# Kernel tuning notes

Hardware: AMD Instinct MI355X
Metric: run time of the kernel (lower is better)

The kernel has to match this reference:

```python
import jax, jax.numpy as jnp
import numpy as np

B, T, C = 2, 2048, 1024
N_HEAD, N_GROUP = 16, 4
N_KV = N_HEAD // N_GROUP          # 4
HEAD_DIM = C // N_HEAD            # 64
ROPE_BASE = 10000.0
INIT_STD = 0.02


def setup_inputs() -> dict:
    key = jax.random.key(0)
    ks = jax.random.split(key, 5)
    kvC = N_KV * HEAD_DIM
    return {
        "x": jax.random.normal(ks[0], (B, T, C), jnp.float32),
        "w_q": jax.random.normal(ks[1], (C, C), jnp.float32) * INIT_STD,
        "b_q": jnp.zeros((C,), jnp.float32),
        "w_k": jax.random.normal(ks[2], (C, kvC), jnp.float32) * INIT_STD,
        "b_k": jnp.zeros((kvC,), jnp.float32),
        "w_v": jax.random.normal(ks[3], (C, kvC), jnp.float32) * INIT_STD,
        "b_v": jnp.zeros((kvC,), jnp.float32),
        "w_o": jax.random.normal(ks[4], (C, C), jnp.float32) * INIT_STD,
        "b_o": jnp.zeros((C,), jnp.float32),
    }


def reference(x, w_q, b_q, w_k, b_k, w_v, b_v, w_o, b_o):
    Bx, Tx, Cx = x.shape
    # projections (torch Linear math with weights stored as [in, out])
    q = (x @ w_q + b_q).reshape(Bx, Tx, N_HEAD, HEAD_DIM).transpose(0, 2, 1, 3)  # [B,H,T,hd]
    k = (x @ w_k + b_k).reshape(Bx, Tx, N_KV, HEAD_DIM).transpose(0, 2, 1, 3)    # [B,KV,T,hd]
    v = (x @ w_v + b_v).reshape(Bx, Tx, N_KV, HEAD_DIM).transpose(0, 2, 1, 3)

    # RoPE with INTERLEAVED pair convention: pairs are (dim 2i, dim 2i+1)
    inv_freq = 1.0 / (ROPE_BASE ** (jnp.arange(0, HEAD_DIM, 2, dtype=jnp.float32) / HEAD_DIM))
    freqs = jnp.arange(Tx, dtype=jnp.float32)[:, None] * inv_freq[None, :]       # [T, hd/2]
    cos, sin = jnp.cos(freqs), jnp.sin(freqs)

    def rope(t):
        tp = t.reshape(*t.shape[:-1], HEAD_DIM // 2, 2)
        e, o = tp[..., 0], tp[..., 1]          # even/odd lanes, [B,h,T,hd/2]
        er = e * cos - o * sin
        orr = e * sin + o * cos
        return jnp.stack([er, orr], axis=-1).reshape(t.shape)

    q, k = rope(q), rope(k)

    # GQA: duplicate each KV head n_group times (consecutively, like repeat_interleave)
    k = jnp.repeat(k, N_GROUP, axis=1)   # [B,H,T,hd]
    v = jnp.repeat(v, N_GROUP, axis=1)

    attn = jnp.einsum('bhqd,bhkd->bhqk', q, k) / np.sqrt(HEAD_DIM).astype(np.float32)
    causal = jnp.tril(jnp.ones((Tx, Tx), bool))
    attn = jnp.where(causal, attn, -jnp.inf)
    attn = jax.nn.softmax(attn, axis=-1)

    out = jnp.einsum('bhqk,bhkd->bhqd', attn, v)            # [B,H,T,hd]
    out = out.transpose(0, 2, 1, 3).reshape(Bx, Tx, Cx)
    return out @ w_o + b_o
```

## Files before the change

### kernel.cpp

```cpp
#include <hip/hip_runtime.h>
#include <hip/hip_bf16.h>

typedef __hip_bfloat16 bf16;
typedef __attribute__((ext_vector_type(8))) short short8_t;
typedef __attribute__((ext_vector_type(4))) short short4_t;
typedef __attribute__((ext_vector_type(4))) float f32x4;

#define B_SZ   2
#define T_SEQ  2048
#define C_DIM  1024
#define NH     16
#define NKV    4
#define HD     64
#define QKVW   1536

#define LOG2_BASE_OVER_32 0.4152410118609203f
#define Q_SCALE 0.1803368801111204f

__device__ __forceinline__ short f2bs(float f) {
    unsigned u = __float_as_uint(f);
    u += 0x7FFFu + ((u >> 16) & 1u);
    return (short)(u >> 16);
}
__device__ __forceinline__ short f2bs_trunc(float f) {
    return (short)(__float_as_uint(f) >> 16);
}
__device__ __forceinline__ float bs2f(short s) {
    unsigned u = ((unsigned)(unsigned short)s) << 16;
    return __uint_as_float(u);
}

__device__ __forceinline__ void store_c(float* p, float v) { *p = v; }
__device__ __forceinline__ void store_c(short* p, float v) { *p = f2bs(v); }

__device__ __forceinline__ float dpp_max16(float x) {
    int t;
    t = __builtin_amdgcn_update_dpp(0, __float_as_int(x), 0xB1, 0xF, 0xF, true);
    x = fmaxf(x, __int_as_float(t));
    t = __builtin_amdgcn_update_dpp(0, __float_as_int(x), 0x4E, 0xF, 0xF, true);
    x = fmaxf(x, __int_as_float(t));
    t = __builtin_amdgcn_update_dpp(0, __float_as_int(x), 0x141, 0xF, 0xF, true);
    x = fmaxf(x, __int_as_float(t));
    t = __builtin_amdgcn_update_dpp(0, __float_as_int(x), 0x140, 0xF, 0xF, true);
    x = fmaxf(x, __int_as_float(t));
    return x;
}

__device__ __forceinline__ void transpose_tile(
    const float* __restrict__ W, short* __restrict__ Wt,
    int K, int N, int n0, int k0, int tid)
{
    __shared__ float tile[32][33];
    int tx = tid & 31, ty = tid >> 5;
    #pragma unroll
    for (int i = 0; i < 4; ++i)
        tile[ty + 8 * i][tx] = W[(size_t)(k0 + ty + 8 * i) * N + n0 + tx];
    __syncthreads();
    #pragma unroll
    for (int i = 0; i < 4; ++i)
        Wt[(size_t)(n0 + ty + 8 * i) * K + k0 + tx] = f2bs(tile[tx][ty + 8 * i]);
}

__global__ __launch_bounds__(256) void prep_kernel(
    const float* __restrict__ x,
    const float* __restrict__ w_q, const float* __restrict__ w_k,
    const float* __restrict__ w_v, const float* __restrict__ w_o,
    const float* __restrict__ b_q, const float* __restrict__ b_k,
    const float* __restrict__ b_v,
    short* __restrict__ Xb, short* __restrict__ Wqkv, short* __restrict__ Wto,
    float* __restrict__ Bqkv, float2* __restrict__ Tab)
{
    int blk = blockIdx.x, tid = threadIdx.x;
    if (blk < 4096) {
        int i = blk * 1024 + tid * 4;
        float4 v = *(const float4*)(x + i);
        short4_t o;
        o[0] = f2bs(v.x); o[1] = f2bs(v.y); o[2] = f2bs(v.z); o[3] = f2bs(v.w);
        *(short4_t*)(Xb + i) = o;
    } else if (blk < 5120) {
        int l = blk - 4096;
        transpose_tile(w_q, Wqkv, C_DIM, C_DIM, (l & 31) * 32, (l >> 5) * 32, tid);
    } else if (blk < 5376) {
        int l = blk - 5120;
        transpose_tile(w_k, Wqkv + (size_t)1024 * C_DIM, C_DIM, 256,
                       (l & 7) * 32, (l >> 3) * 32, tid);
    } else if (blk < 5632) {
        int l = blk - 5376;
        transpose_tile(w_v, Wqkv + (size_t)1280 * C_DIM, C_DIM, 256,
                       (l & 7) * 32, (l >> 3) * 32, tid);
    } else if (blk < 6656) {
        int l = blk - 5632;
        transpose_tile(w_o, Wto, C_DIM, C_DIM, (l & 31) * 32, (l >> 5) * 32, tid);
    } else if (blk < 6662) {
        int i = (blk - 6656) * 256 + tid;
        float v;
        if (i < 1024)      v = b_q[i];
        else if (i < 1280) v = b_k[i - 1024];
        else               v = b_v[i - 1280];
        Bqkv[i] = v;
    } else {
        int idx = (blk - 6662) * 256 + tid;
        int t = idx >> 5, i = idx & 31;
        float ang = (float)t * exp2f(-(float)i * LOG2_BASE_OVER_32);
        Tab[idx] = make_float2(cosf(ang), sinf(ang));
    }
}

template <typename CT>
__global__ __launch_bounds__(256) void gemm_mfma_bt(
    const short* __restrict__ A, const short* __restrict__ Bt,
    const float* __restrict__ bias, CT* __restrict__ C,
    int M, int N, int K)
{
    __shared__ __align__(16) short sA[2][128][40];
    __shared__ __align__(16) short sB[2][128][40];

    int m0 = blockIdx.y * 128;
    int n0 = blockIdx.x * 128;
    int tid  = threadIdx.x;
    int w    = tid >> 6, lane = tid & 63;
    int quad = lane >> 4, l16 = lane & 15;
    int wm = w & 1, wn = w >> 1;

    f32x4 acc[4][4] = {};

    short8_t ra[2], rb[2];
    #pragma unroll
    for (int it = 0; it < 2; ++it) {
        int slot = tid + 256 * it, row = slot >> 2, g = (slot & 3) * 8;
        ra[it] = *(const short8_t*)(A  + (size_t)(m0 + row) * K + g);
        rb[it] = *(const short8_t*)(Bt + (size_t)(n0 + row) * K + g);
    }

    int buf = 0;
    for (int k0 = 0; k0 < K; k0 += 32, buf ^= 1) {
        #pragma unroll
        for (int it = 0; it < 2; ++it) {
            int slot = tid + 256 * it, row = slot >> 2, g = (slot & 3) * 8;
            *(short8_t*)&sA[buf][row][g] = ra[it];
            *(short8_t*)&sB[buf][row][g] = rb[it];
        }
        if (k0 + 32 < K) {
            #pragma unroll
            for (int it = 0; it < 2; ++it) {
                int slot = tid + 256 * it, row = slot >> 2, g = (slot & 3) * 8;
                ra[it] = *(const short8_t*)(A  + (size_t)(m0 + row) * K + k0 + 32 + g);
                rb[it] = *(const short8_t*)(Bt + (size_t)(n0 + row) * K + k0 + 32 + g);
            }
        }
        __syncthreads();

        short8_t af[4], bfr[4];
        #pragma unroll
        for (int mt = 0; mt < 4; ++mt)
            af[mt] = *(const short8_t*)&sA[buf][wm * 64 + mt * 16 + l16][quad * 8];
        #pragma unroll
        for (int nt = 0; nt < 4; ++nt)
            bfr[nt] = *(const short8_t*)&sB[buf][wn * 64 + nt * 16 + l16][quad * 8];
        #pragma unroll
        for (int mt = 0; mt < 4; ++mt)
            #pragma unroll
            for (int nt = 0; nt < 4; ++nt)
                acc[mt][nt] = __builtin_amdgcn_mfma_f32_16x16x32_bf16(
                    af[mt], bfr[nt], acc[mt][nt], 0, 0, 0);
    }

    #pragma unroll
    for (int mt = 0; mt < 4; ++mt) {
        #pragma unroll
        for (int nt = 0; nt < 4; ++nt) {
            int col = n0 + wn * 64 + nt * 16 + l16;
            float bv = bias[col];
            #pragma unroll
            for (int r = 0; r < 4; ++r) {
                int row = m0 + wm * 64 + mt * 16 + quad * 4 + r;
                store_c(&C[(size_t)row * N + col], acc[mt][nt][r] + bv);
            }
        }
    }
}

__global__ __launch_bounds__(256) void rope_k_kernel(
    short* __restrict__ QKV, const float2* __restrict__ Tab)
{
    int g = blockIdx.x * 256 + threadIdx.x;
    int row = g >> 7, pi = g & 127;
    int col = 1024 + pi * 2;
    int t = row & (T_SEQ - 1);
    int i = pi & 31;

    size_t base = (size_t)row * QKVW + col;
    float e = bs2f(QKV[base]);
    float o = bs2f(QKV[base + 1]);

    float2 cs = Tab[t * 32 + i];

    QKV[base]     = f2bs(e * cs.x - o * cs.y);
    QKV[base + 1] = f2bs(e * cs.y + o * cs.x);
}

__global__ __launch_bounds__(256) void attn_mfma5(
    const short* __restrict__ QKV, const float2* __restrict__ Tab,
    short* __restrict__ O)
{
    __shared__ __align__(16) short sK [64][72];
    __shared__ __align__(16) short sVt[64][72];
    __shared__ __align__(16) short sP [4][16][72];

    const int tid  = threadIdx.x;
    const int w    = tid >> 6;
    const int lane = tid & 63;
    const int quad = lane >> 4;
    const int l16  = lane & 15;

    int blk = blockIdx.x;
    int grp = blk & 7;
    int tq  = 127 - (blk >> 3);
    int kvh = grp & 3;
    int b   = grp >> 2;
    int h   = kvh * 4 + w;
    int ct  = tq >> 2;

    const short* qptr = QKV + ((size_t)(b * T_SEQ + tq * 16 + l16)) * QKVW + h * HD;
    short8_t q0r = *(const short8_t*)(qptr + quad * 8);
    short8_t q1r = *(const short8_t*)(qptr + quad * 8 + 32);
    int t = tq * 16 + l16;
    const float2* tb = Tab + t * 32 + quad * 4;
    short8_t qf0, qf1;
    #pragma unroll
    for (int j = 0; j < 4; ++j) {
        float2 cs0 = tb[j];
        float e0 = bs2f(q0r[2 * j]), o0 = bs2f(q0r[2 * j + 1]);
        qf0[2 * j]     = f2bs((e0 * cs0.x - o0 * cs0.y) * Q_SCALE);
        qf0[2 * j + 1] = f2bs((e0 * cs0.y + o0 * cs0.x) * Q_SCALE);
        float2 cs1 = tb[j + 16];
        float e1 = bs2f(q1r[2 * j]), o1 = bs2f(q1r[2 * j + 1]);
        qf1[2 * j]     = f2bs((e1 * cs1.x - o1 * cs1.y) * Q_SCALE);
        qf1[2 * j + 1] = f2bs((e1 * cs1.y + o1 * cs1.x) * Q_SCALE);
    }

    const short* kbase = QKV + (size_t)b * T_SEQ * QKVW + 1024 + kvh * HD;
    const short* vbase = QKV + (size_t)b * T_SEQ * QKVW + 1280 + kvh * HD;

    short8_t ones;
    #pragma unroll
    for (int i = 0; i < 8; ++i) ones[i] = (short)0x3F80;

    float mrow[4], lrow[4];
    f32x4 oacc[4];
    #pragma unroll
    for (int r = 0; r < 4; ++r) { mrow[r] = -INFINITY; lrow[r] = 0.f; }
    #pragma unroll
    for (int dt = 0; dt < 4; ++dt) oacc[dt] = (f32x4){0.f, 0.f, 0.f, 0.f};

    const int kkey = tid >> 3, kd = (tid & 7) * 8;
    const int vkey = tid & 63, vd = (tid >> 6) * 8;

    short8_t kr[2], vr[2];
    #pragma unroll
    for (int it = 0; it < 2; ++it) {
        kr[it] = *(const short8_t*)(kbase + (size_t)(kkey + 32 * it) * QKVW + kd);
        vr[it] = *(const short8_t*)(vbase + (size_t)vkey * QKVW + vd + 32 * it);
    }

    for (int c = 0; c <= ct; ++c) {
        __syncthreads();
        #pragma unroll
        for (int it = 0; it < 2; ++it) {
            *(short8_t*)&sK[kkey + 32 * it][kd] = kr[it];
            #pragma unroll
            for (int i = 0; i < 8; ++i) sVt[vd + 32 * it + i][vkey] = vr[it][i];
        }
        __syncthreads();
        if (c < ct) {
            int jn = (c + 1) * 64;
            #pragma unroll
            for (int it = 0; it < 2; ++it) {
                kr[it] = *(const short8_t*)(kbase + (size_t)(jn + kkey + 32 * it) * QKVW + kd);
                vr[it] = *(const short8_t*)(vbase + (size_t)(jn + vkey) * QKVW + vd + 32 * it);
            }
        }

        f32x4 sacc[4];
        #pragma unroll
        for (int nt = 0; nt < 4; ++nt) {
            f32x4 z = {0.f, 0.f, 0.f, 0.f};
            short8_t kf0 = *(const short8_t*)&sK[l16 + 16 * nt][quad * 8];
            short8_t kf1 = *(const short8_t*)&sK[l16 + 16 * nt][quad * 8 + 32];
            z = __builtin_amdgcn_mfma_f32_16x16x32_bf16(qf0, kf0, z, 0, 0, 0);
            z = __builtin_amdgcn_mfma_f32_16x16x32_bf16(qf1, kf1, z, 0, 0, 0);
            sacc[nt] = z;
        }

        bool maskc = (c == ct);
        int j0 = c * 64;
        float al[4];
        #pragma unroll
        for (int r = 0; r < 4; ++r) {
            int trow = tq * 16 + quad * 4 + r;
            float sv[4], vmax = -INFINITY;
            #pragma unroll
            for (int nt = 0; nt < 4; ++nt) {
                float s = sacc[nt][r];
                if (maskc && (j0 + 16 * nt + l16 > trow)) s = -INFINITY;
                sv[nt] = s;
                vmax = fmaxf(vmax, s);
            }
            vmax = dpp_max16(vmax);
            float mnew = fmaxf(mrow[r], vmax);
            al[r] = exp2f(mrow[r] - mnew);
            mrow[r] = mnew;
            #pragma unroll
            for (int nt = 0; nt < 4; ++nt)
                sP[w][quad * 4 + r][16 * nt + l16] = f2bs_trunc(exp2f(sv[nt] - mnew));
        }
        if (__any((al[0] < 1.f) || (al[1] < 1.f) || (al[2] < 1.f) || (al[3] < 1.f))) {
            #pragma unroll
            for (int r = 0; r < 4; ++r) lrow[r] *= al[r];
            #pragma unroll
            for (int dt = 0; dt < 4; ++dt) {
                f32x4 o = oacc[dt];
                o[0] *= al[0]; o[1] *= al[1]; o[2] *= al[2]; o[3] *= al[3];
                oacc[dt] = o;
            }
        }

        short8_t pf0 = *(const short8_t*)&sP[w][l16][quad * 8];
        short8_t pf1 = *(const short8_t*)&sP[w][l16][quad * 8 + 32];
        f32x4 rs = {0.f, 0.f, 0.f, 0.f};
        rs = __builtin_amdgcn_mfma_f32_16x16x32_bf16(pf0, ones, rs, 0, 0, 0);
        rs = __builtin_amdgcn_mfma_f32_16x16x32_bf16(pf1, ones, rs, 0, 0, 0);
        #pragma unroll
        for (int r = 0; r < 4; ++r) lrow[r] += rs[r];
        #pragma unroll
        for (int dt = 0; dt < 4; ++dt) {
            short8_t vf0 = *(const short8_t*)&sVt[l16 + 16 * dt][quad * 8];
            short8_t vf1 = *(const short8_t*)&sVt[l16 + 16 * dt][quad * 8 + 32];
            oacc[dt] = __builtin_amdgcn_mfma_f32_16x16x32_bf16(pf0, vf0, oacc[dt], 0, 0, 0);
            oacc[dt] = __builtin_amdgcn_mfma_f32_16x16x32_bf16(pf1, vf1, oacc[dt], 0, 0, 0);
        }
    }

    #pragma unroll
    for (int r = 0; r < 4; ++r) {
        int m = quad * 4 + r;
        float inv = __builtin_amdgcn_rcpf(lrow[r]);
        #pragma unroll
        for (int dt = 0; dt < 4; ++dt)
            O[((size_t)b * T_SEQ + tq * 16 + m) * C_DIM + h * HD + 16 * dt + l16] =
                f2bs(oacc[dt][r] * inv);
    }
}

extern "C" void kernel_launch(void* const* d_in, const int* in_sizes, int n_in,
                              void* d_out, int out_size, void* d_ws, size_t ws_size,
                              hipStream_t stream)
{
    const float* x   = (const float*)d_in[0];
    const float* w_q = (const float*)d_in[1];
    const float* b_q = (const float*)d_in[2];
    const float* w_k = (const float*)d_in[3];
    const float* b_k = (const float*)d_in[4];
    const float* w_v = (const float*)d_in[5];
    const float* b_v = (const float*)d_in[6];
    const float* w_o = (const float*)d_in[7];
    const float* b_o = (const float*)d_in[8];
    float* out = (float*)d_out;

    char* ws = (char*)d_ws;
    short*  Xb   = (short*) (ws);
    short*  Ab   = (short*) (ws + ((size_t)8  << 20));
    short*  QKVb = (short*) (ws + ((size_t)16 << 20));
    short*  Wqkv = (short*) (ws + ((size_t)28 << 20));
    short*  Wto  = (short*) (ws + ((size_t)31 << 20));
    float*  Bqkv = (float*) (ws + ((size_t)33 << 20));
    float2* Tab  = (float2*)(ws + ((size_t)33 << 20) + 8192);

    const int M = B_SZ * T_SEQ;

    prep_kernel<<<6918, 256, 0, stream>>>(
        x, w_q, w_k, w_v, w_o, b_q, b_k, b_v, Xb, Wqkv, Wto, Bqkv, Tab);

    gemm_mfma_bt<short><<<dim3(QKVW / 128, M / 128), 256, 0, stream>>>(
        Xb, Wqkv, Bqkv, QKVb, M, QKVW, C_DIM);

    rope_k_kernel<<<2048, 256, 0, stream>>>(QKVb, Tab);

    attn_mfma5<<<B_SZ * NKV * 128, 256, 0, stream>>>(QKVb, Tab, Ab);

    gemm_mfma_bt<float><<<dim3(C_DIM / 128, M / 128), 256, 0, stream>>>(
        Ab, Wto, b_o, out, M, C_DIM, C_DIM);
}
```

Measured before the change: 190.3 us.

## Pre-transpose V globally and compute transposed scores to simplify softmax

The RoPE-K kernel now also writes a transposed copy of V to workspace. The attention kernel can then fill its V tile in shared memory with plain vector stores instead of scalar transposing writes. The score MFMA swaps its operands so each lane holds one query's scores across keys. This makes the row max and sum a two-step shuffle per lane, and removes the ones-vector MFMA row sum and the DPP reductions. In exchange it adds an extra global V transpose pass and cross-lane shuffles to broadcast the rescale factors.

```diff
diff --git a/kernel.cpp b/kernel.cpp
--- a/kernel.cpp
+++ b/kernel.cpp
@@ -32,19 +32,6 @@
 
 __device__ __forceinline__ void store_c(float* p, float v) { *p = v; }
 __device__ __forceinline__ void store_c(short* p, float v) { *p = f2bs(v); }
-
-__device__ __forceinline__ float dpp_max16(float x) {
-    int t;
-    t = __builtin_amdgcn_update_dpp(0, __float_as_int(x), 0xB1, 0xF, 0xF, true);
-    x = fmaxf(x, __int_as_float(t));
-    t = __builtin_amdgcn_update_dpp(0, __float_as_int(x), 0x4E, 0xF, 0xF, true);
-    x = fmaxf(x, __int_as_float(t));
-    t = __builtin_amdgcn_update_dpp(0, __float_as_int(x), 0x141, 0xF, 0xF, true);
-    x = fmaxf(x, __int_as_float(t));
-    t = __builtin_amdgcn_update_dpp(0, __float_as_int(x), 0x140, 0xF, 0xF, true);
-    x = fmaxf(x, __int_as_float(t));
-    return x;
-}
 
 __device__ __forceinline__ void transpose_tile(
     const float* __restrict__ W, short* __restrict__ Wt,
@@ -180,28 +167,50 @@
     }
 }
 
-__global__ __launch_bounds__(256) void rope_k_kernel(
-    short* __restrict__ QKV, const float2* __restrict__ Tab)
-{
-    int g = blockIdx.x * 256 + threadIdx.x;
-    int row = g >> 7, pi = g & 127;
-    int col = 1024 + pi * 2;
-    int t = row & (T_SEQ - 1);
-    int i = pi & 31;
-
-    size_t base = (size_t)row * QKVW + col;
-    float e = bs2f(QKV[base]);
-    float o = bs2f(QKV[base + 1]);
-
-    float2 cs = Tab[t * 32 + i];
-
-    QKV[base]     = f2bs(e * cs.x - o * cs.y);
-    QKV[base + 1] = f2bs(e * cs.y + o * cs.x);
-}
-
-__global__ __launch_bounds__(256) void attn_mfma5(
-    const short* __restrict__ QKV, const float2* __restrict__ Tab,
-    short* __restrict__ O)
+__global__ __launch_bounds__(256) void rope_k_transpose_v(
+    short* __restrict__ QKV, const float2* __restrict__ Tab,
+    short* __restrict__ Vt)
+{
+    int blk = blockIdx.x, tid = threadIdx.x;
+    if (blk < 2048) {
+        int g = blk * 256 + tid;
+        int row = g >> 7, pi = g & 127;
+        int col = 1024 + pi * 2;
+        int t = row & (T_SEQ - 1);
+        int i = pi & 31;
+        size_t base = (size_t)row * QKVW + col;
+        float e = bs2f(QKV[base]);
+        float o = bs2f(QKV[base + 1]);
+        float2 cs = Tab[t * 32 + i];
+        QKV[base]     = f2bs(e * cs.x - o * cs.y);
+        QKV[base + 1] = f2bs(e * cs.y + o * cs.x);
+    } else {
+        __shared__ __align__(16) short sT[64][72];
+        int l = blk - 2048;
+        int d0 = (l >> 6) * 64;
+        int r0 = (l & 63) * 64;
+        int i0 = tid >> 3, seg = (tid & 7) * 8;
+        #pragma unroll
+        for (int it = 0; it < 2; ++it) {
+            int i = i0 + 32 * it;
+            *(short8_t*)&sT[i][seg] =
+                *(const short8_t*)(QKV + (size_t)(r0 + i) * QKVW + 1280 + d0 + seg);
+        }
+        __syncthreads();
+        #pragma unroll
+        for (int it = 0; it < 2; ++it) {
+            int d = i0 + 32 * it;
+            short8_t o;
+            #pragma unroll
+            for (int k = 0; k < 8; ++k) o[k] = sT[seg + k][d];
+            *(short8_t*)(Vt + (size_t)(d0 + d) * (B_SZ * T_SEQ) + r0 + seg) = o;
+        }
+    }
+}
+
+__global__ __launch_bounds__(256) void attn_mfma6(
+    const short* __restrict__ QKV, const short* __restrict__ Vt,
+    const float2* __restrict__ Tab, short* __restrict__ O)
 {
     __shared__ __align__(16) short sK [64][72];
     __shared__ __align__(16) short sVt[64][72];
@@ -224,8 +233,8 @@
     const short* qptr = QKV + ((size_t)(b * T_SEQ + tq * 16 + l16)) * QKVW + h * HD;
     short8_t q0r = *(const short8_t*)(qptr + quad * 8);
     short8_t q1r = *(const short8_t*)(qptr + quad * 8 + 32);
-    int t = tq * 16 + l16;
-    const float2* tb = Tab + t * 32 + quad * 4;
+    int tg = tq * 16 + l16;
+    const float2* tb = Tab + tg * 32 + quad * 4;
     short8_t qf0, qf1;
     #pragma unroll
     for (int j = 0; j < 4; ++j) {
@@ -239,37 +248,30 @@
         qf1[2 * j + 1] = f2bs((e1 * cs1.y + o1 * cs1.x) * Q_SCALE);
     }
 
-    const short* kbase = QKV + (size_t)b * T_SEQ * QKVW + 1024 + kvh * HD;
-    const short* vbase = QKV + (size_t)b * T_SEQ * QKVW + 1280 + kvh * HD;
-
-    short8_t ones;
-    #pragma unroll
-    for (int i = 0; i < 8; ++i) ones[i] = (short)0x3F80;
-
-    float mrow[4], lrow[4];
+    const short* kbase  = QKV + (size_t)b * T_SEQ * QKVW + 1024 + kvh * HD;
+    const short* vtbase = Vt + (size_t)(kvh * HD) * (B_SZ * T_SEQ) + b * T_SEQ;
+
+    float m_l = -INFINITY, l_l = 0.f;
     f32x4 oacc[4];
     #pragma unroll
-    for (int r = 0; r < 4; ++r) { mrow[r] = -INFINITY; lrow[r] = 0.f; }
-    #pragma unroll
     for (int dt = 0; dt < 4; ++dt) oacc[dt] = (f32x4){0.f, 0.f, 0.f, 0.f};
 
     const int kkey = tid >> 3, kd = (tid & 7) * 8;
-    const int vkey = tid & 63, vd = (tid >> 6) * 8;
+    const int vdim = tid >> 3, vseg = (tid & 7) * 8;
 
     short8_t kr[2], vr[2];
     #pragma unroll
     for (int it = 0; it < 2; ++it) {
         kr[it] = *(const short8_t*)(kbase + (size_t)(kkey + 32 * it) * QKVW + kd);
-        vr[it] = *(const short8_t*)(vbase + (size_t)vkey * QKVW + vd + 32 * it);
+        vr[it] = *(const short8_t*)(vtbase + (size_t)(vdim + 32 * it) * (B_SZ * T_SEQ) + vseg);
     }
 
     for (int c = 0; c <= ct; ++c) {
         __syncthreads();
         #pragma unroll
         for (int it = 0; it < 2; ++it) {
-            *(short8_t*)&sK[kkey + 32 * it][kd] = kr[it];
-            #pragma unroll
-            for (int i = 0; i < 8; ++i) sVt[vd + 32 * it + i][vkey] = vr[it][i];
+            *(short8_t*)&sK [kkey + 32 * it][kd]   = kr[it];
+            *(short8_t*)&sVt[vdim + 32 * it][vseg] = vr[it];
         }
         __syncthreads();
         if (c < ct) {
@@ -277,65 +279,72 @@
             #pragma unroll
             for (int it = 0; it < 2; ++it) {
                 kr[it] = *(const short8_t*)(kbase + (size_t)(jn + kkey + 32 * it) * QKVW + kd);
-                vr[it] = *(const short8_t*)(vbase + (size_t)(jn + vkey) * QKVW + vd + 32 * it);
+                vr[it] = *(const short8_t*)(vtbase + (size_t)(vdim + 32 * it) * (B_SZ * T_SEQ) + jn + vseg);
             }
         }
 
         f32x4 sacc[4];
         #pragma unroll
-        for (int nt = 0; nt < 4; ++nt) {
+        for (int kt = 0; kt < 4; ++kt) {
             f32x4 z = {0.f, 0.f, 0.f, 0.f};
-            short8_t kf0 = *(const short8_t*)&sK[l16 + 16 * nt][quad * 8];
-            short8_t kf1 = *(const short8_t*)&sK[l16 + 16 * nt][quad * 8 + 32];
-            z = __builtin_amdgcn_mfma_f32_16x16x32_bf16(qf0, kf0, z, 0, 0, 0);
-            z = __builtin_amdgcn_mfma_f32_16x16x32_bf16(qf1, kf1, z, 0, 0, 0);
-            sacc[nt] = z;
-        }
-
-        bool maskc = (c == ct);
-        int j0 = c * 64;
-        float al[4];
-        #pragma unroll
-        for (int r = 0; r < 4; ++r) {
-            int trow = tq * 16 + quad * 4 + r;
-            float sv[4], vmax = -INFINITY;
-            #pragma unroll
-            for (int nt = 0; nt < 4; ++nt) {
-                float s = sacc[nt][r];
-                if (maskc && (j0 + 16 * nt + l16 > trow)) s = -INFINITY;
-                sv[nt] = s;
-                vmax = fmaxf(vmax, s);
+            short8_t kf0 = *(const short8_t*)&sK[l16 + 16 * kt][quad * 8];
+            short8_t kf1 = *(const short8_t*)&sK[l16 + 16 * kt][quad * 8 + 32];
+            z = __builtin_amdgcn_mfma_f32_16x16x32_bf16(kf0, qf0, z, 0, 0, 0);
+            z = __builtin_amdgcn_mfma_f32_16x16x32_bf16(kf1, qf1, z, 0, 0, 0);
+            sacc[kt] = z;
+        }
+
+        if (c == ct) {
+            int j0 = c * 64;
+            #pragma unroll
+            for (int kt = 0; kt < 4; ++kt)
+                #pragma unroll
+                for (int r = 0; r < 4; ++r)
+                    if (j0 + 16 * kt + quad * 4 + r > tg) sacc[kt][r] = -INFINITY;
+        }
+
+        float vmax = sacc[0][0];
+        #pragma unroll
+        for (int kt = 0; kt < 4; ++kt)
+            #pragma unroll
+            for (int r = 0; r < 4; ++r) vmax = fmaxf(vmax, sacc[kt][r]);
+        vmax = fmaxf(vmax, __shfl_xor(vmax, 16));
+        vmax = fmaxf(vmax, __shfl_xor(vmax, 32));
+        float mnew = fmaxf(m_l, vmax);
+        float al = exp2f(m_l - mnew);
+        m_l = mnew;
+
+        float psum = 0.f;
+        #pragma unroll
+        for (int kt = 0; kt < 4; ++kt) {
+            short4_t pk;
+            #pragma unroll
+            for (int r = 0; r < 4; ++r) {
+                float p = exp2f(sacc[kt][r] - mnew);
+                psum += p;
+                pk[r] = f2bs_trunc(p);
             }
-            vmax = dpp_max16(vmax);
-            float mnew = fmaxf(mrow[r], vmax);
-            al[r] = exp2f(mrow[r] - mnew);
-            mrow[r] = mnew;
-            #pragma unroll
-            for (int nt = 0; nt < 4; ++nt)
-                sP[w][quad * 4 + r][16 * nt + l16] = f2bs_trunc(exp2f(sv[nt] - mnew));
-        }
-        if (__any((al[0] < 1.f) || (al[1] < 1.f) || (al[2] < 1.f) || (al[3] < 1.f))) {
-            #pragma unroll
-            for (int r = 0; r < 4; ++r) lrow[r] *= al[r];
-            #pragma unroll
-            for (int dt = 0; dt < 4; ++dt) {
-                f32x4 o = oacc[dt];
-                o[0] *= al[0]; o[1] *= al[1]; o[2] *= al[2]; o[3] *= al[3];
-                oacc[dt] = o;
+            *(short4_t*)&sP[w][l16][16 * kt + 4 * quad] = pk;
+        }
+        psum += __shfl_xor(psum, 16);
+        psum += __shfl_xor(psum, 32);
+        l_l = l_l * al + psum;
+
+        if (__any(al < 1.f)) {
+            #pragma unroll
+            for (int r = 0; r < 4; ++r) {
+                float alr = __shfl(al, quad * 4 + r);
+                #pragma unroll
+                for (int dt = 0; dt < 4; ++dt) oacc[dt][r] *= alr;
             }
         }
 
         short8_t pf0 = *(const short8_t*)&sP[w][l16][quad * 8];
         short8_t pf1 = *(const short8_t*)&sP[w][l16][quad * 8 + 32];
-        f32x4 rs = {0.f, 0.f, 0.f, 0.f};
-        rs = __builtin_amdgcn_mfma_f32_16x16x32_bf16(pf0, ones, rs, 0, 0, 0);
-        rs = __builtin_amdgcn_mfma_f32_16x16x32_bf16(pf1, ones, rs, 0, 0, 0);
-        #pragma unroll
-        for (int r = 0; r < 4; ++r) lrow[r] += rs[r];
         #pragma unroll
         for (int dt = 0; dt < 4; ++dt) {
-            short8_t vf0 = *(const short8_t*)&sVt[l16 + 16 * dt][quad * 8];
-            short8_t vf1 = *(const short8_t*)&sVt[l16 + 16 * dt][quad * 8 + 32];
+            short8_t vf0 = *(const short8_t*)&sVt[16 * dt + l16][quad * 8];
+            short8_t vf1 = *(const short8_t*)&sVt[16 * dt + l16][quad * 8 + 32];
             oacc[dt] = __builtin_amdgcn_mfma_f32_16x16x32_bf16(pf0, vf0, oacc[dt], 0, 0, 0);
             oacc[dt] = __builtin_amdgcn_mfma_f32_16x16x32_bf16(pf1, vf1, oacc[dt], 0, 0, 0);
         }
@@ -344,7 +353,8 @@
     #pragma unroll
     for (int r = 0; r < 4; ++r) {
         int m = quad * 4 + r;
-        float inv = __builtin_amdgcn_rcpf(lrow[r]);
+        float lr = __shfl(l_l, quad * 4 + r);
+        float inv = __builtin_amdgcn_rcpf(lr);
         #pragma unroll
         for (int dt = 0; dt < 4; ++dt)
             O[((size_t)b * T_SEQ + tq * 16 + m) * C_DIM + h * HD + 16 * dt + l16] =
@@ -375,6 +385,7 @@
     short*  Wto  = (short*) (ws + ((size_t)31 << 20));
     float*  Bqkv = (float*) (ws + ((size_t)33 << 20));
     float2* Tab  = (float2*)(ws + ((size_t)33 << 20) + 8192);
+    short*  Vt   = (short*) (ws + ((size_t)34 << 20));
 
     const int M = B_SZ * T_SEQ;
 
@@ -384,9 +395,9 @@
     gemm_mfma_bt<short><<<dim3(QKVW / 128, M / 128), 256, 0, stream>>>(
         Xb, Wqkv, Bqkv, QKVb, M, QKVW, C_DIM);
 
-    rope_k_kernel<<<2048, 256, 0, stream>>>(QKVb, Tab);
-
-    attn_mfma5<<<B_SZ * NKV * 128, 256, 0, stream>>>(QKVb, Tab, Ab);
+    rope_k_transpose_v<<<2304, 256, 0, stream>>>(QKVb, Tab, Vt);
+
+    attn_mfma6<<<B_SZ * NKV * 128, 256, 0, stream>>>(QKVb, Vt, Tab, Ab);
 
     gemm_mfma_bt<float><<<dim3(C_DIM / 128, M / 128), 256, 0, stream>>>(
         Ab, Wto, b_o, out, M, C_DIM, C_DIM);
```

After: 181.5 us. 1.05x faster.
